# Kernel tuning notes

Hardware: AMD Instinct MI355X
Metric: run time of the kernel (lower is better)

Reference implementation:

```python
import math
import jax, jax.numpy as jnp
import numpy as np

V, D, H, L, F, S, B = 32000, 768, 12, 6, 3072, 2048, 4
DK = D // H


def setup_inputs() -> dict:
    key = jax.random.key(0)
    ks = jax.random.split(key, 16)
    sc = 0.02
    n = jax.random.normal
    inp = {
        "input_ids": jax.random.randint(ks[0], (B, S), 0, V, dtype=jnp.int64)
        if jax.config.jax_enable_x64 else jax.random.randint(ks[0], (B, S), 0, V, dtype=jnp.int32),
        "emb": n(ks[1], (V, D), jnp.float32) * sc,
        "Wq": n(ks[2], (L, D, D), jnp.float32) * sc, "bq": jnp.zeros((L, D), jnp.float32),
        "Wk": n(ks[3], (L, D, D), jnp.float32) * sc, "bk": jnp.zeros((L, D), jnp.float32),
        "Wv": n(ks[4], (L, D, D), jnp.float32) * sc, "bv": jnp.zeros((L, D), jnp.float32),
        "Wo": n(ks[5], (L, D, D), jnp.float32) * sc, "bo": jnp.zeros((L, D), jnp.float32),
        "W1": n(ks[6], (L, D, F), jnp.float32) * sc, "b1": jnp.zeros((L, F), jnp.float32),
        "W2": n(ks[7], (L, F, D), jnp.float32) * sc, "b2": jnp.zeros((L, D), jnp.float32),
        "gamma": jnp.ones((L, D), jnp.float32), "beta": jnp.zeros((L, D), jnp.float32),
    }
    return inp


def _pos_encoding(seq_len, d):
    pos = jnp.arange(seq_len, dtype=jnp.float32)[:, None]                  # [S,1]
    div = jnp.exp(jnp.arange(0, d, 2, dtype=jnp.float32) * (-math.log(10000.0) / d))
    ang = pos * div                                                        # [S,D/2]
    return jnp.stack([jnp.sin(ang), jnp.cos(ang)], axis=-1).reshape(seq_len, d)


def _layernorm(x, g, b, eps=1e-5):
    mu = x.mean(-1, keepdims=True)
    var = ((x - mu) ** 2).mean(-1, keepdims=True)
    return (x - mu) * jax.lax.rsqrt(var + eps) * g + b


def _forward(input_ids, emb, Wq, bq, Wk, bk, Wv, bv, Wo, bo, W1, b1, W2, b2, gamma, beta):
    mask = (input_ids != 1)[:, None, None, :]                              # [B,1,1,S]
    x = emb[input_ids] + _pos_encoding(input_ids.shape[1], emb.shape[1])   # [B,S,D]

    def layer(x, p):
        wq, bq_, wk, bk_, wv, bv_, wo, bo_, w1, b1_, w2, b2_, g, bt = p
        def heads(h):  # [B,S,D] -> [B,H,S,DK]
            return h.reshape(B, S, H, DK).transpose(0, 2, 1, 3)
        q = heads(x @ wq + bq_)
        k = heads(x @ wk + bk_)
        v = heads(x @ wv + bv_)
        scores = jnp.einsum("bhqd,bhkd->bhqk", q, k) / math.sqrt(DK)
        scores = jnp.where(mask, scores, -1e9)
        attn = jax.nn.softmax(scores, axis=-1)
        o = jnp.einsum("bhqk,bhkd->bhqd", attn, v)
        o = o.transpose(0, 2, 1, 3).reshape(B, S, D) @ wo + bo_
        x1 = _layernorm(x + o, g, bt)
        ff = jax.nn.relu(x1 @ w1 + b1_) @ w2 + b2_
        return _layernorm(x1 + ff, g, bt), None  # same norm params reused (as in source)

    x, _ = jax.lax.scan(layer, x, (Wq, bq, Wk, bk, Wv, bv, Wo, bo, W1, b1, W2, b2, gamma, beta))
    return x.mean(axis=1)                                                  # [B,D]


def reference(input_ids, emb, Wq, bq, Wk, bk, Wv, bv, Wo, bo, W1, b1, W2, b2, gamma, beta):
    return _forward(input_ids, emb, Wq, bq, Wk, bk, Wv, bv, Wo, bo, W1, b1, W2, b2, gamma, beta)
```

## Files before the change

### kernel.cpp

```cpp
#include <hip/hip_runtime.h>
#include <hip/hip_bf16.h>
#include <math.h>

typedef unsigned short u16;
typedef unsigned long long u64;
using bf16x8 = __attribute__((ext_vector_type(8))) short;
using f32x4  = __attribute__((ext_vector_type(4))) float;

static constexpr int kD = 768;
static constexpr int kH = 12;
static constexpr int kL = 6;
static constexpr int kF = 3072;
static constexpr int kS = 2048;
static constexpr int kB = 4;
static constexpr int kQW = 2304;
static constexpr int kNT = kB * kS;

__device__ __forceinline__ u16 f2bf(float f) {
    return __bfloat16_as_ushort(__float2bfloat16(f));
}

__device__ __forceinline__ unsigned cvtpk(float a, float b) {
    unsigned d;
    asm volatile("v_cvt_pk_bf16_f32 %0, %1, %2" : "=v"(d) : "v"(a), "v"(b));
    return d;
}

__device__ __forceinline__ void gload16(const void* g, void* l) {
    auto gp = reinterpret_cast<const __attribute__((address_space(1))) unsigned int*>(
        reinterpret_cast<uintptr_t>(g));
    auto lp = reinterpret_cast<__attribute__((address_space(3))) unsigned int*>(
        reinterpret_cast<uintptr_t>(l));
    __builtin_amdgcn_global_load_lds(gp, lp, 16, 0, 0);
}

__global__ __launch_bounds__(256) void embed_pe(
    const int* __restrict__ ids, const float* __restrict__ emb,
    float* __restrict__ x, u16* __restrict__ xbf)
{
    const int t = blockIdx.x;
    const int s = t & (kS - 1);
    const int id = ids[t];
#pragma unroll
    for (int j = 0; j < 3; ++j) {
        const int d = threadIdx.x + (j << 8);
        const float i2 = (float)((d >> 1) << 1);
        const float dv = __expf(i2 * (-9.210340371976184f / 768.f));
        const float ang = (float)s * dv;
        const float pe = (d & 1) ? cosf(ang) : sinf(ang);
        const float v = emb[(size_t)id * kD + d] + pe;
        x[(size_t)t * kD + d] = v;
        if (xbf) xbf[(size_t)t * kD + d] = f2bf(v);
    }
}

__global__ __launch_bounds__(64) void mk_maskbits(const int* __restrict__ ids,
                                                  u64* __restrict__ mbits)
{
    const int w = blockIdx.x;
    const int lane = threadIdx.x;
    const u64 m = __ballot(ids[(size_t)w * 64 + lane] != 1);
    if (lane == 0) mbits[w] = m;
}

__global__ __launch_bounds__(256) void bias_build(
    const float* __restrict__ bq, const float* __restrict__ bk,
    const float* __restrict__ bv, const float* __restrict__ bo,
    const float* __restrict__ b1, const float* __restrict__ b2,
    float* __restrict__ ba)
{
    const int i = blockIdx.x * 256 + threadIdx.x;
    if (i >= 6 * 6912) return;
    const int l = i / 6912, p = i % 6912;
    float v;
    if      (p < 768)  v = bq[l * 768 + p] * 0.125f;
    else if (p < 1536) v = bk[l * 768 + p - 768];
    else if (p < 2304) v = bv[l * 768 + p - 1536];
    else if (p < 3072) v = bo[l * 768 + p - 2304];
    else if (p < 6144) v = b1[(size_t)l * 3072 + p - 3072];
    else               v = b2[l * 768 + p - 6144];
    ba[i] = v;
}

static constexpr size_t OFF_WO = (size_t)2304 * 768;
static constexpr size_t OFF_W1 = OFF_WO + (size_t)768 * 768;
static constexpr size_t OFF_W2 = OFF_W1 + (size_t)3072 * 768;
static constexpr size_t WARENA_E = OFF_W2 + (size_t)768 * 3072;

__global__ __launch_bounds__(256) void cvt_all(
    const float* __restrict__ Wq, const float* __restrict__ Wk,
    const float* __restrict__ Wv, const float* __restrict__ Wo,
    const float* __restrict__ W1, const float* __restrict__ W2,
    u16* __restrict__ wa)
{
    __shared__ float T[64][68];
    const int t = blockIdx.x;
    const float* S; u16* Dp; int Nsrc, Kdst, srow0, scol0; float sc = 1.f;
    if (t < 432) {
        const int ni = t % 36, ki = t / 36;
        const int ng = ni * 64;
        const int sel = ng / 768;
        scol0 = ng % 768; srow0 = ki * 64;
        S = (sel == 0) ? Wq : (sel == 1) ? Wk : Wv;
        if (sel == 0) sc = 0.125f;
        Nsrc = 768; Kdst = 768;
        Dp = wa + (size_t)ng * 768 + srow0;
    } else if (t < 576) {
        const int tt = t - 432; const int ni = tt % 12, ki = tt / 12;
        scol0 = ni * 64; srow0 = ki * 64;
        S = Wo; Nsrc = 768; Kdst = 768;
        Dp = wa + OFF_WO + (size_t)(ni * 64) * 768 + srow0;
    } else if (t < 1152) {
        const int tt = t - 576; const int ni = tt % 48, ki = tt / 48;
        scol0 = ni * 64; srow0 = ki * 64;
        S = W1; Nsrc = 3072; Kdst = 768;
        Dp = wa + OFF_W1 + (size_t)(ni * 64) * 768 + srow0;
    } else {
        const int tt = t - 1152; const int ni = tt % 12, ki = tt / 12;
        scol0 = ni * 64; srow0 = ki * 64;
        S = W2; Nsrc = 768; Kdst = 3072;
        Dp = wa + OFF_W2 + (size_t)(ni * 64) * 3072 + srow0;
    }
    const int tid = threadIdx.x;
#pragma unroll
    for (int i = 0; i < 4; ++i) {
        const int idx = tid + (i << 8);
        const int kr = idx >> 4;
        const int nc = (idx & 15) << 2;
        const float4 v = *(const float4*)(S + (size_t)(srow0 + kr) * Nsrc + scol0 + nc);
        T[kr][nc] = v.x; T[kr][nc + 1] = v.y; T[kr][nc + 2] = v.z; T[kr][nc + 3] = v.w;
    }
    __syncthreads();
#pragma unroll
    for (int i = 0; i < 4; ++i) {
        const int idx = tid + (i << 8);
        const int nr = idx >> 4;
        const int kc = (idx & 15) << 2;
        ushort4 o;
        o.x = f2bf(T[kc][nr] * sc);     o.y = f2bf(T[kc + 1][nr] * sc);
        o.z = f2bf(T[kc + 2][nr] * sc); o.w = f2bf(T[kc + 3][nr] * sc);
        *(ushort4*)(Dp + (size_t)nr * Kdst + kc) = o;
    }
}

__global__ __launch_bounds__(256) void gemm_bf16(
    const u16* __restrict__ A, const u16* __restrict__ Bt,
    const float* __restrict__ bias, void* __restrict__ Cv,
    u16* __restrict__ vTp, int M, int N, int K, int mode)
{
    __shared__ u16 As[2][4096];
    __shared__ u16 Bs[2][4096];
    const int tid = threadIdx.x;
    const int l = tid & 63;
    const int lo = l & 15, hi = l >> 4;
    const int w = tid >> 6, wr = w >> 1, wc = w & 1;

    int brow = blockIdx.x, bcol = blockIdx.y;
    const int gx = gridDim.x;
    if ((gx & 7) == 0) {
        const int id = blockIdx.y * gx + blockIdx.x;
        const int xcd = id & 7, idx = id >> 3;
        const int rpx = gx >> 3;
        brow = xcd * rpx + (idx % rpx);
        bcol = idx / rpx;
    }
    const size_t row0 = (size_t)brow * 128;
    const size_t col0 = (size_t)bcol * 128;

    const int c0 = tid, c1 = tid + 256;
    const int r0 = c0 >> 2, g0 = (c0 & 3) ^ ((r0 >> 1) & 3);
    const int r1 = c1 >> 2, g1 = (c1 & 3) ^ ((r1 >> 1) & 3);
    const u16* a0 = A  + (row0 + r0) * K + g0 * 8;
    const u16* a1 = A  + (row0 + r1) * K + g1 * 8;
    const u16* b0 = Bt + (col0 + r0) * K + g0 * 8;
    const u16* b1 = Bt + (col0 + r1) * K + g1 * 8;

    f32x4 acc[4][4];
#pragma unroll
    for (int i = 0; i < 4; ++i)
#pragma unroll
        for (int j = 0; j < 4; ++j)
#pragma unroll
            for (int r = 0; r < 4; ++r) acc[i][j][r] = 0.f;

    int aoff[4], boff[4];
#pragma unroll
    for (int i = 0; i < 4; ++i) {
        const int ra = wr * 64 + i * 16 + lo;
        aoff[i] = ra * 32 + ((hi ^ ((ra >> 1) & 3)) << 3);
        const int rb = wc * 64 + i * 16 + lo;
        boff[i] = rb * 32 + ((hi ^ ((rb >> 1) & 3)) << 3);
    }

    const int NT = K >> 5;
    gload16(a0, As[0] + c0 * 8);
    gload16(a1, As[0] + c1 * 8);
    gload16(b0, Bs[0] + c0 * 8);
    gload16(b1, Bs[0] + c1 * 8);

    int cur = 0;
    for (int t = 0; t < NT; ++t) {
        if (t + 1 < NT) {
            const int k0 = (t + 1) << 5;
            const int nb = cur ^ 1;
            gload16(a0 + k0, As[nb] + c0 * 8);
            gload16(a1 + k0, As[nb] + c1 * 8);
            gload16(b0 + k0, Bs[nb] + c0 * 8);
            gload16(b1 + k0, Bs[nb] + c1 * 8);
            asm volatile("s_waitcnt vmcnt(4)" ::: "memory");
        } else {
            asm volatile("s_waitcnt vmcnt(0)" ::: "memory");
        }
        __builtin_amdgcn_s_barrier();
        bf16x8 af[4], bfr[4];
#pragma unroll
        for (int i = 0; i < 4; ++i) af[i]  = *(const bf16x8*)&As[cur][aoff[i]];
#pragma unroll
        for (int j = 0; j < 4; ++j) bfr[j] = *(const bf16x8*)&Bs[cur][boff[j]];
#pragma unroll
        for (int i = 0; i < 4; ++i)
#pragma unroll
            for (int j = 0; j < 4; ++j)
                acc[i][j] = __builtin_amdgcn_mfma_f32_16x16x32_bf16(
                    af[i], bfr[j], acc[i][j], 0, 0, 0);
        asm volatile("s_waitcnt lgkmcnt(0)" ::: "memory");
        __builtin_amdgcn_sched_barrier(0);
        __builtin_amdgcn_s_barrier();
        cur ^= 1;
    }

    const bool vmode = (mode == 3) && (col0 >= 1536);
    if (vmode) {
#pragma unroll
        for (int i = 0; i < 4; ++i) {
            const size_t rbase = row0 + wr * 64 + i * 16 + hi * 4;
            const size_t tb = (rbase >> 6) * 64;
            const int k0 = (int)(rbase & 63);
            const int pos = (((k0 >> 2) & 3) << 3) + (((k0 >> 4) & 1) << 2)
                          + ((k0 >> 5) << 5);
#pragma unroll
            for (int j = 0; j < 4; ++j) {
                const size_t c = col0 + wc * 64 + j * 16 + lo;
                const float bs = bias[c];
                const size_t d = c - 1536;
                ushort4 o;
                o.x = f2bf(acc[i][j][0] + bs);
                o.y = f2bf(acc[i][j][1] + bs);
                o.z = f2bf(acc[i][j][2] + bs);
                o.w = f2bf(acc[i][j][3] + bs);
                *(ushort4*)(vTp + d * (size_t)M + tb + pos) = o;
            }
        }
        return;
    }

#pragma unroll
    for (int i = 0; i < 4; ++i) {
        const size_t rbase = row0 + wr * 64 + i * 16 + hi * 4;
#pragma unroll
        for (int j = 0; j < 4; ++j) {
            const size_t c = col0 + wc * 64 + j * 16 + lo;
            const float bs = bias[c];
#pragma unroll
            for (int r = 0; r < 4; ++r) {
                float v = acc[i][j][r] + bs;
                if (mode == 2) v = fmaxf(v, 0.f);
                const size_t off = (rbase + r) * (size_t)N + c;
                if (mode == 0) ((float*)Cv)[off] = v;
                else           ((u16*)Cv)[off]  = f2bf(v);
            }
        }
    }
}

__global__ __launch_bounds__(256) void attn_mfma(
    const u16* __restrict__ QKV, const u16* __restrict__ vT,
    const u64* __restrict__ mbits, u16* __restrict__ O)
{
    __shared__ u16 Ks[2][4096];
    __shared__ u16 Vs[2][4096];

    const int tid = threadIdx.x, l = tid & 63, w = tid >> 6;
    const int lo = l & 15, hi = l >> 4;
    const int h = blockIdx.y, b = blockIdx.z;
    const int q0 = blockIdx.x << 6;

    bf16x8 qf0, qf1;
    {
        const u16* qp = QKV + ((size_t)(b * kS + q0 + w * 16 + lo)) * kQW
                            + h * 64 + hi * 8;
        qf0 = *(const bf16x8*)qp;
        qf1 = *(const bf16x8*)(qp + 32);
    }

    const int ga = tid, gb = tid + 256;
    const int rwA = ga >> 3, sxA = ga & 7, EA = sxA ^ (rwA & 7);
    const int rwB = gb >> 3, sxB = gb & 7, EB = sxB ^ (rwB & 7);
    const u16* Kbase = QKV + (size_t)(b * kS) * kQW + 768 + h * 64;
    const u16* Vbase = vT + (size_t)(h * 64) * kNT + b * kS;

    f32x4 accO[4];
#pragma unroll
    for (int n = 0; n < 4; ++n)
#pragma unroll
        for (int r = 0; r < 4; ++r) accO[n][r] = 0.f;
    float m = -3.0e38f, lsum = 0.f;

    const int ksw = (lo & 7) << 3;
    constexpr int NTt = kS / 64;

    gload16(Kbase + (size_t)rwA * kQW + EA * 8, Ks[0] + ga * 8);
    gload16(Kbase + (size_t)rwB * kQW + EB * 8, Ks[0] + gb * 8);
    gload16(Vbase + (size_t)rwA * kNT + EA * 8, Vs[0] + ga * 8);
    gload16(Vbase + (size_t)rwB * kNT + EB * 8, Vs[0] + gb * 8);

    int cur = 0;
    for (int kt = 0; kt < NTt; ++kt) {
        asm volatile("s_waitcnt vmcnt(0)" ::: "memory");
        __syncthreads();

        if (kt + 1 < NTt) {
            const size_t kof = (size_t)((kt + 1) << 6) * kQW;
            const size_t vof = (size_t)((kt + 1) << 6);
            u16* kd = Ks[cur ^ 1];
            u16* vd = Vs[cur ^ 1];
            gload16(Kbase + kof + (size_t)rwA * kQW + EA * 8, kd + ga * 8);
            gload16(Kbase + kof + (size_t)rwB * kQW + EB * 8, kd + gb * 8);
            gload16(Vbase + (size_t)rwA * kNT + vof + EA * 8, vd + ga * 8);
            gload16(Vbase + (size_t)rwB * kNT + vof + EB * 8, vd + gb * 8);
        }

        f32x4 st[4];
        __builtin_amdgcn_s_setprio(1);
#pragma unroll
        for (int j = 0; j < 4; ++j) {
#pragma unroll
            for (int r = 0; r < 4; ++r) st[j][r] = 0.f;
            const int kb2 = (j * 16 + lo) * 64;
            const bf16x8 k0 = *(const bf16x8*)&Ks[cur][kb2 + ((hi * 8)      ^ ksw)];
            const bf16x8 k1 = *(const bf16x8*)&Ks[cur][kb2 + ((hi * 8 + 32) ^ ksw)];
            st[j] = __builtin_amdgcn_mfma_f32_16x16x32_bf16(k0, qf0, st[j], 0, 0, 0);
            st[j] = __builtin_amdgcn_mfma_f32_16x16x32_bf16(k1, qf1, st[j], 0, 0, 0);
        }
        __builtin_amdgcn_s_setprio(0);

        float rmax = st[0][0];
#pragma unroll
        for (int j = 0; j < 4; ++j)
#pragma unroll
            for (int r = 0; r < 4; ++r) rmax = fmaxf(rmax, st[j][r]);
        rmax = fmaxf(rmax, __shfl_xor(rmax, 16));
        rmax = fmaxf(rmax, __shfl_xor(rmax, 32));

        const bool skip = __all(rmax <= m + 8.0f);
        if (!skip) {
            const float mn = fmaxf(m, rmax);
            const float corr = __expf(m - mn);
            m = mn;
            lsum *= corr;
            float c2[4];
#pragma unroll
            for (int r = 0; r < 4; ++r) c2[r] = __shfl(corr, hi * 4 + r);
#pragma unroll
            for (int n = 0; n < 4; ++n)
#pragma unroll
                for (int r = 0; r < 4; ++r) accO[n][r] *= c2[r];
        }

#pragma unroll
        for (int j = 0; j < 4; ++j)
#pragma unroll
            for (int r = 0; r < 4; ++r) st[j][r] = __expf(st[j][r] - m);

        const u64 mb = mbits[b * 32 + kt];
        if (mb != ~0ull) {
#pragma unroll
            for (int j = 0; j < 4; ++j)
#pragma unroll
                for (int r = 0; r < 4; ++r)
                    if (!((mb >> (j * 16 + hi * 4 + r)) & 1)) st[j][r] = 0.f;
        }

        float ts = 0.f;
#pragma unroll
        for (int j = 0; j < 4; ++j)
#pragma unroll
            for (int r = 0; r < 4; ++r) ts += st[j][r];
        ts += __shfl_xor(ts, 16);
        ts += __shfl_xor(ts, 32);
        lsum += ts;

        union PU { unsigned u[4]; bf16x8 v; } p0, p1;
        p0.u[0] = cvtpk(st[0][0], st[0][1]); p0.u[1] = cvtpk(st[0][2], st[0][3]);
        p0.u[2] = cvtpk(st[1][0], st[1][1]); p0.u[3] = cvtpk(st[1][2], st[1][3]);
        p1.u[0] = cvtpk(st[2][0], st[2][1]); p1.u[1] = cvtpk(st[2][2], st[2][3]);
        p1.u[2] = cvtpk(st[3][0], st[3][1]); p1.u[3] = cvtpk(st[3][2], st[3][3]);

        __builtin_amdgcn_s_setprio(1);
#pragma unroll
        for (int n = 0; n < 4; ++n) {
            const int vb2 = (n * 16 + lo) * 64;
            const bf16x8 v0 = *(const bf16x8*)&Vs[cur][vb2 + ((hi * 8)      ^ ksw)];
            const bf16x8 v1 = *(const bf16x8*)&Vs[cur][vb2 + ((hi * 8 + 32) ^ ksw)];
            accO[n] = __builtin_amdgcn_mfma_f32_16x16x32_bf16(p0.v, v0, accO[n], 0, 0, 0);
            accO[n] = __builtin_amdgcn_mfma_f32_16x16x32_bf16(p1.v, v1, accO[n], 0, 0, 0);
        }
        __builtin_amdgcn_s_setprio(0);
        cur ^= 1;
    }

    float linv[4];
#pragma unroll
    for (int r = 0; r < 4; ++r) linv[r] = 1.f / __shfl(lsum, hi * 4 + r);
#pragma unroll
    for (int n = 0; n < 4; ++n)
#pragma unroll
        for (int r = 0; r < 4; ++r)
            O[((size_t)(b * kS + q0 + w * 16 + hi * 4 + r)) * kD
              + h * 64 + n * 16 + lo] = f2bf(accO[n][r] * linv[r]);
}

__global__ __launch_bounds__(256) void add_ln(
    const float* __restrict__ a, const float* __restrict__ r,
    const float* __restrict__ g, const float* __restrict__ bt,
    float* __restrict__ out, u16* __restrict__ outb)
{
    const int lane = threadIdx.x & 63;
    const size_t row = (size_t)blockIdx.x * 4 + (threadIdx.x >> 6);
    const float4* a4 = (const float4*)(a + row * kD);
    const float4* r4 = (const float4*)(r + row * kD);
    float4 v[3];
    float s = 0.f;
#pragma unroll
    for (int j = 0; j < 3; ++j) {
        const float4 av = a4[j * 64 + lane];
        const float4 rv = r4[j * 64 + lane];
        v[j].x = av.x + rv.x; v[j].y = av.y + rv.y;
        v[j].z = av.z + rv.z; v[j].w = av.w + rv.w;
        s += v[j].x + v[j].y + v[j].z + v[j].w;
    }
#pragma unroll
    for (int off = 32; off; off >>= 1) s += __shfl_xor(s, off);
    const float mu = s * (1.f / 768.f);
    float vs = 0.f;
#pragma unroll
    for (int j = 0; j < 3; ++j) {
        float t0 = v[j].x - mu, t1 = v[j].y - mu, t2 = v[j].z - mu, t3 = v[j].w - mu;
        vs = fmaf(t0, t0, fmaf(t1, t1, fmaf(t2, t2, fmaf(t3, t3, vs))));
    }
#pragma unroll
    for (int off = 32; off; off >>= 1) vs += __shfl_xor(vs, off);
    const float rstd = rsqrtf(vs * (1.f / 768.f) + 1e-5f);
    const float4* g4 = (const float4*)g;
    const float4* b4 = (const float4*)bt;
#pragma unroll
    for (int j = 0; j < 3; ++j) {
        const float4 gv = g4[j * 64 + lane];
        const float4 bv = b4[j * 64 + lane];
        float4 o;
        o.x = (v[j].x - mu) * rstd * gv.x + bv.x;
        o.y = (v[j].y - mu) * rstd * gv.y + bv.y;
        o.z = (v[j].z - mu) * rstd * gv.z + bv.z;
        o.w = (v[j].w - mu) * rstd * gv.w + bv.w;
        ((float4*)(out + row * kD))[j * 64 + lane] = o;
        if (outb) {
            ushort4 ob4;
            ob4.x = f2bf(o.x); ob4.y = f2bf(o.y);
            ob4.z = f2bf(o.z); ob4.w = f2bf(o.w);
            ((ushort4*)(outb + row * kD))[j * 64 + lane] = ob4;
        }
    }
}

__global__ __launch_bounds__(256) void mean_part(
    const float* __restrict__ x, float* __restrict__ mred)
{
    const int c = blockIdx.x, b = blockIdx.y;
    const int tid = threadIdx.x;
    const float* base = x + ((size_t)b * kS + c * 32) * kD;
#pragma unroll
    for (int j = 0; j < 3; ++j) {
        const int d = tid + (j << 8);
        float s = 0.f;
#pragma unroll 8
        for (int t = 0; t < 32; ++t) s += base[(size_t)t * kD + d];
        mred[((size_t)b * 64 + c) * kD + d] = s;
    }
}

__global__ __launch_bounds__(256) void mean_fin(
    const float* __restrict__ mred, float* __restrict__ out)
{
    const int d = blockIdx.x * 256 + threadIdx.x;
    const int b = blockIdx.y;
    float s = 0.f;
#pragma unroll
    for (int c = 0; c < 64; ++c) s += mred[((size_t)b * 64 + c) * kD + d];
    out[b * kD + d] = s * (1.f / 2048.f);
}

__global__ __launch_bounds__(256) void mean_s(
    const float* __restrict__ x, float* __restrict__ out)
{
    const int d = blockIdx.x * 256 + threadIdx.x;
    const int b = blockIdx.y;
    float s = 0.f;
    for (int t = 0; t < kS; ++t) s += x[((size_t)b * kS + t) * kD + d];
    out[b * kD + d] = s * (1.f / 2048.f);
}

__global__ __launch_bounds__(256) void gemm_f32(
    const float* __restrict__ A, const float* __restrict__ W,
    const float* __restrict__ bias, float* __restrict__ C,
    int M, int N, int K, int relu)
{
    __shared__ float As[16][68];
    __shared__ float Bs[16][68];
    const int tid = threadIdx.x;
    const int row0 = blockIdx.x << 6;
    const int col0 = blockIdx.y << 6;
    const int tx = tid & 15, ty = tid >> 4;
    const int ar = tid >> 2;
    const int ak = (tid & 3) << 2;
    const int bk = tid >> 4;
    const int bc = (tid & 15) << 2;
    float acc[4][4] = {};
    const float* Ap = A + (size_t)(row0 + ar) * K + ak;
    const float* Wp = W + (size_t)bk * N + col0 + bc;
    for (int k0 = 0; k0 < K; k0 += 16) {
        const float4 a4 = *(const float4*)(Ap + k0);
        const float4 b4 = *(const float4*)(Wp + (size_t)k0 * N);
        __syncthreads();
        As[ak + 0][ar] = a4.x; As[ak + 1][ar] = a4.y;
        As[ak + 2][ar] = a4.z; As[ak + 3][ar] = a4.w;
        *(float4*)&Bs[bk][bc] = b4;
        __syncthreads();
#pragma unroll
        for (int kk = 0; kk < 16; ++kk) {
            const float4 av = *(const float4*)&As[kk][ty << 2];
            const float4 bv = *(const float4*)&Bs[kk][tx << 2];
            const float aa[4] = {av.x, av.y, av.z, av.w};
            const float bb[4] = {bv.x, bv.y, bv.z, bv.w};
#pragma unroll
            for (int i = 0; i < 4; ++i)
#pragma unroll
                for (int j = 0; j < 4; ++j)
                    acc[i][j] = fmaf(aa[i], bb[j], acc[i][j]);
        }
    }
#pragma unroll
    for (int i = 0; i < 4; ++i) {
        const int row = row0 + (ty << 2) + i;
#pragma unroll
        for (int j = 0; j < 4; ++j) {
            const int col = col0 + (tx << 2) + j;
            float v = acc[i][j] + bias[col];
            if (relu) v = fmaxf(v, 0.f);
            C[(size_t)row * N + col] = v;
        }
    }
}

__global__ __launch_bounds__(256) void attn_fused(
    const float* __restrict__ Q, const float* __restrict__ Km,
    const float* __restrict__ Vm, const int* __restrict__ ids,
    float* __restrict__ O)
{
    __shared__ float Ksf[64 * 64];
    __shared__ float Vtf[64 * 64];
    __shared__ float Qs[16][64];
    __shared__ float Psf[4][4][64];
    const int tid = threadIdx.x;
    const int w = tid >> 6;
    const int lane = tid & 63;
    const int h = blockIdx.y, b = blockIdx.z;
    const int qrow0 = blockIdx.x << 4;
    {
        const int r = tid >> 4;
        const int c4 = tid & 15;
        const float4 q4 = *(const float4*)(
            Q + ((size_t)(b * kS + qrow0 + r)) * kD + h * 64 + (c4 << 2));
        Qs[r][(c4 << 2) + 0] = q4.x * 0.125f;
        Qs[r][(c4 << 2) + 1] = q4.y * 0.125f;
        Qs[r][(c4 << 2) + 2] = q4.z * 0.125f;
        Qs[r][(c4 << 2) + 3] = q4.w * 0.125f;
    }
    float m[4], lsum[4], o[4];
#pragma unroll
    for (int r = 0; r < 4; ++r) { m[r] = -3.0e38f; lsum[r] = 0.f; o[r] = 0.f; }
    for (int kt = 0; kt < kS / 64; ++kt) {
        __syncthreads();
#pragma unroll
        for (int i = 0; i < 4; ++i) {
            const int lin = tid + (i << 8);
            const int row = lin >> 4;
            const int s4 = lin & 15;
            const size_t gro = ((size_t)(b * kS + (kt << 6) + row)) * kD + h * 64 + (s4 << 2);
            const float4 k4 = *(const float4*)(Km + gro);
            ((float4*)Ksf)[(row << 4) + (s4 ^ (row & 7))] = k4;
            const float4 v4 = *(const float4*)(Vm + gro);
            const int ksl = row >> 2, ke = row & 3;
            const int d0 = s4 << 2;
            Vtf[(d0 + 0) * 64 + ((ksl ^ ((d0 + 0) & 7)) << 2) + ke] = v4.x;
            Vtf[(d0 + 1) * 64 + ((ksl ^ ((d0 + 1) & 7)) << 2) + ke] = v4.y;
            Vtf[(d0 + 2) * 64 + ((ksl ^ ((d0 + 2) & 7)) << 2) + ke] = v4.z;
            Vtf[(d0 + 3) * 64 + ((ksl ^ ((d0 + 3) & 7)) << 2) + ke] = v4.w;
        }
        __syncthreads();
        const bool masked = (ids[(size_t)b * kS + (kt << 6) + lane] == 1);
        float scr[4] = {0.f, 0.f, 0.f, 0.f};
#pragma unroll
        for (int i16 = 0; i16 < 16; ++i16) {
            const float4 kv = ((const float4*)Ksf)[(lane << 4) + (i16 ^ (lane & 7))];
#pragma unroll
            for (int r = 0; r < 4; ++r) {
                const float4 qv = *(const float4*)&Qs[(w << 2) + r][i16 << 2];
                scr[r] = fmaf(kv.x, qv.x, fmaf(kv.y, qv.y,
                          fmaf(kv.z, qv.z, fmaf(kv.w, qv.w, scr[r]))));
            }
        }
#pragma unroll
        for (int r = 0; r < 4; ++r) {
            float sm = masked ? -3.0e38f : scr[r];
#pragma unroll
            for (int off = 32; off; off >>= 1) sm = fmaxf(sm, __shfl_xor(sm, off));
            const float mn = fmaxf(m[r], sm);
            const float cr = __expf(m[r] - mn);
            const float pv = masked ? 0.f : __expf(scr[r] - mn);
            float ps = pv;
#pragma unroll
            for (int off = 32; off; off >>= 1) ps += __shfl_xor(ps, off);
            lsum[r] = lsum[r] * cr + ps;
            o[r] *= cr;
            m[r] = mn;
            Psf[w][r][lane] = pv;
        }
#pragma unroll
        for (int i16 = 0; i16 < 16; ++i16) {
            const float4 vv = ((const float4*)Vtf)[(lane << 4) + (i16 ^ (lane & 7))];
#pragma unroll
            for (int r = 0; r < 4; ++r) {
                const float4 pv = *(const float4*)&Psf[w][r][i16 << 2];
                o[r] = fmaf(pv.x, vv.x, fmaf(pv.y, vv.y,
                        fmaf(pv.z, vv.z, fmaf(pv.w, vv.w, o[r]))));
            }
        }
    }
#pragma unroll
    for (int r = 0; r < 4; ++r)
        O[((size_t)(b * kS + qrow0 + (w << 2) + r)) * kD + h * 64 + lane] =
            o[r] / lsum[r];
}

extern "C" void kernel_launch(void* const* d_in, const int* in_sizes, int n_in,
                              void* d_out, int out_size, void* d_ws, size_t ws_size,
                              hipStream_t stream)
{
    const int*   ids   = (const int*)  d_in[0];
    const float* emb   = (const float*)d_in[1];
    const float* Wq    = (const float*)d_in[2];
    const float* bq    = (const float*)d_in[3];
    const float* Wk    = (const float*)d_in[4];
    const float* bk    = (const float*)d_in[5];
    const float* Wv    = (const float*)d_in[6];
    const float* bv    = (const float*)d_in[7];
    const float* Wo    = (const float*)d_in[8];
    const float* bo    = (const float*)d_in[9];
    const float* W1    = (const float*)d_in[10];
    const float* b1    = (const float*)d_in[11];
    const float* W2    = (const float*)d_in[12];
    const float* b2    = (const float*)d_in[13];
    const float* gamma = (const float*)d_in[14];
    const float* beta  = (const float*)d_in[15];
    float* out = (float*)d_out;

    const size_t BUFE = (size_t)kB * kS * kD;
    const size_t WDD  = (size_t)kD * kD;
    const size_t WDF  = (size_t)kD * kF;
    const size_t HIDE = (size_t)kB * kS * kF;
    const int NTOK = kB * kS;

    const size_t NEED = BUFE * 4 * 2
                      + BUFE * 2
                      + HIDE * 2
                      + WARENA_E * 2
                      + (size_t)6 * 6912 * 4
                      + 128 * 8
                      + (size_t)kB * 64 * kD * 4;

    if (ws_size >= NEED) {
        float* xb  = (float*)d_ws;
        float* ob  = xb + BUFE;
        u16*   abf = (u16*)(ob + BUFE);
        u16*   sc  = abf + BUFE;
        u16*   vtb = sc + (size_t)NTOK * kQW;
        u16*   wa  = sc + HIDE;
        float* ba  = (float*)(wa + WARENA_E);
        u64*   mbt = (u64*)(ba + 6 * 6912);
        float* mrd = (float*)(mbt + 128);

        embed_pe<<<NTOK, 256, 0, stream>>>(ids, emb, xb, abf);
        mk_maskbits<<<kB * kS / 64, 64, 0, stream>>>(ids, mbt);
        bias_build<<<(6 * 6912 + 255) / 256, 256, 0, stream>>>(
            bq, bk, bv, bo, b1, b2, ba);

        for (int l = 0; l < kL; ++l) {
            const size_t oDD = (size_t)l * WDD;
            const size_t oDF = (size_t)l * WDF;
            const float* bl = ba + (size_t)l * 6912;
            const float* gl  = gamma + (size_t)l * kD;
            const float* btl = beta  + (size_t)l * kD;

            cvt_all<<<1728, 256, 0, stream>>>(
                Wq + oDD, Wk + oDD, Wv + oDD, Wo + oDD, W1 + oDF, W2 + oDF, wa);

            gemm_bf16<<<dim3(64, 18), 256, 0, stream>>>(
                abf, wa, bl, sc, vtb, NTOK, kQW, kD, 3);

            attn_mfma<<<dim3(kS / 64, kH, kB), 256, 0, stream>>>(
                sc, vtb, mbt, abf);

            gemm_bf16<<<dim3(64, 6), 256, 0, stream>>>(
                abf, wa + OFF_WO, bl + 2304, ob, nullptr, NTOK, kD, kD, 0);

            add_ln<<<NTOK / 4, 256, 0, stream>>>(xb, ob, gl, btl, ob, abf);

            gemm_bf16<<<dim3(64, 24), 256, 0, stream>>>(
                abf, wa + OFF_W1, bl + 3072, sc, nullptr, NTOK, kF, kD, 2);
            gemm_bf16<<<dim3(64, 6), 256, 0, stream>>>(
                sc, wa + OFF_W2, bl + 6144, xb, nullptr, NTOK, kD, kF, 0);

            add_ln<<<NTOK / 4, 256, 0, stream>>>(ob, xb, gl, btl, xb, abf);
        }

        mean_part<<<dim3(64, kB), 256, 0, stream>>>(xb, mrd);
        mean_fin<<<dim3(kD / 256, kB), 256, 0, stream>>>(mrd, out);
        return;
    }

    if (ws_size < 5 * BUFE * sizeof(float)) return;
    float* xb = (float*)d_ws;
    float* kb = xb + BUFE;
    float* qb = kb + BUFE;
    float* vb = qb + BUFE;
    float* obf = vb + BUFE;
    float* hb = qb;

    embed_pe<<<NTOK, 256, 0, stream>>>(ids, emb, xb, nullptr);
    for (int l = 0; l < kL; ++l) {
        const size_t oDD = (size_t)l * WDD;
        const size_t oDF = (size_t)l * WDF;
        gemm_f32<<<dim3(NTOK / 64, kD / 64), 256, 0, stream>>>(
            xb, Wq + oDD, bq + (size_t)l * kD, qb, NTOK, kD, kD, 0);
        gemm_f32<<<dim3(NTOK / 64, kD / 64), 256, 0, stream>>>(
            xb, Wk + oDD, bk + (size_t)l * kD, kb, NTOK, kD, kD, 0);
        gemm_f32<<<dim3(NTOK / 64, kD / 64), 256, 0, stream>>>(
            xb, Wv + oDD, bv + (size_t)l * kD, vb, NTOK, kD, kD, 0);
        attn_fused<<<dim3(kS / 16, kH, kB), 256, 0, stream>>>(qb, kb, vb, ids, obf);
        gemm_f32<<<dim3(NTOK / 64, kD / 64), 256, 0, stream>>>(
            obf, Wo + oDD, bo + (size_t)l * kD, qb, NTOK, kD, kD, 0);
        add_ln<<<NTOK / 4, 256, 0, stream>>>(xb, qb,
            gamma + (size_t)l * kD, beta + (size_t)l * kD, kb, nullptr);
        for (int c = 0; c < 2; ++c) {
            const size_t ro = (size_t)c * 4096;
            gemm_f32<<<dim3(4096 / 64, kF / 64), 256, 0, stream>>>(
                kb + ro * kD, W1 + oDF, b1 + (size_t)l * kF, hb, 4096, kF, kD, 1);
            gemm_f32<<<dim3(4096 / 64, kD / 64), 256, 0, stream>>>(
                hb, W2 + oDF, b2 + (size_t)l * kD, obf + ro * kD, 4096, kD, kF, 0);
        }
        add_ln<<<NTOK / 4, 256, 0, stream>>>(kb, obf,
            gamma + (size_t)l * kD, beta + (size_t)l * kD, xb, nullptr);
    }
    mean_s<<<dim3(kD / 256, kB), 256, 0, stream>>>(xb, out);
}
```

Measured before the change: 1.757 ms.

## Keep residual stream in bf16 and use exp2 softmax with folded log2e scale

The fast path now holds the residual stream, the GEMM outputs and the LayerNorm inputs and outputs in bf16 instead of fp32, which cuts global memory traffic in add_ln and in the Wo/W2 GEMM epilogues. The 1/sqrt(dk)*log2(e) factor is folded into Wq/bq so attention can use a native exp2 instead of expf, and the rescale-skip threshold is widened to match the base-2 domain. Keeping the residual in bf16 accumulates rounding error across six layers and may hurt accuracy against the fp32 reference.

New measurement: 1.662 ms. -5.4%, faster.

```diff
diff --git a/kernel.cpp b/kernel.cpp
--- a/kernel.cpp
+++ b/kernel.cpp
@@ -16,14 +16,25 @@
 static constexpr int kQW = 2304;
 static constexpr int kNT = kB * kS;
 
+static constexpr float kQScale = 0.18033688011112043f;
+
 __device__ __forceinline__ u16 f2bf(float f) {
     return __bfloat16_as_ushort(__float2bfloat16(f));
 }
-
+__device__ __forceinline__ float b2f(u16 u) {
+    return __uint_as_float((unsigned)u << 16);
+}
 __device__ __forceinline__ unsigned cvtpk(float a, float b) {
     unsigned d;
     asm volatile("v_cvt_pk_bf16_f32 %0, %1, %2" : "=v"(d) : "v"(a), "v"(b));
     return d;
+}
+__device__ __forceinline__ float exp2fast(float x) {
+#if __has_builtin(__builtin_amdgcn_exp2f)
+    return __builtin_amdgcn_exp2f(x);
+#else
+    return __expf(x * 0.6931471805599453f);
+#endif
 }
 
 __device__ __forceinline__ void gload16(const void* g, void* l) {
@@ -36,7 +47,7 @@
 
 __global__ __launch_bounds__(256) void embed_pe(
     const int* __restrict__ ids, const float* __restrict__ emb,
-    float* __restrict__ x, u16* __restrict__ xbf)
+    u16* __restrict__ xbf)
 {
     const int t = blockIdx.x;
     const int s = t & (kS - 1);
@@ -48,9 +59,25 @@
         const float dv = __expf(i2 * (-9.210340371976184f / 768.f));
         const float ang = (float)s * dv;
         const float pe = (d & 1) ? cosf(ang) : sinf(ang);
-        const float v = emb[(size_t)id * kD + d] + pe;
-        x[(size_t)t * kD + d] = v;
-        if (xbf) xbf[(size_t)t * kD + d] = f2bf(v);
+        xbf[(size_t)t * kD + d] = f2bf(emb[(size_t)id * kD + d] + pe);
+    }
+}
+
+__global__ __launch_bounds__(256) void embed_pe_f32(
+    const int* __restrict__ ids, const float* __restrict__ emb,
+    float* __restrict__ x)
+{
+    const int t = blockIdx.x;
+    const int s = t & (kS - 1);
+    const int id = ids[t];
+#pragma unroll
+    for (int j = 0; j < 3; ++j) {
+        const int d = threadIdx.x + (j << 8);
+        const float i2 = (float)((d >> 1) << 1);
+        const float dv = __expf(i2 * (-9.210340371976184f / 768.f));
+        const float ang = (float)s * dv;
+        const float pe = (d & 1) ? cosf(ang) : sinf(ang);
+        x[(size_t)t * kD + d] = emb[(size_t)id * kD + d] + pe;
     }
 }
 
@@ -73,7 +100,7 @@
     if (i >= 6 * 6912) return;
     const int l = i / 6912, p = i % 6912;
     float v;
-    if      (p < 768)  v = bq[l * 768 + p] * 0.125f;
+    if      (p < 768)  v = bq[l * 768 + p] * kQScale;
     else if (p < 1536) v = bk[l * 768 + p - 768];
     else if (p < 2304) v = bv[l * 768 + p - 1536];
     else if (p < 3072) v = bo[l * 768 + p - 2304];
@@ -102,7 +129,7 @@
         const int sel = ng / 768;
         scol0 = ng % 768; srow0 = ki * 64;
         S = (sel == 0) ? Wq : (sel == 1) ? Wk : Wv;
-        if (sel == 0) sc = 0.125f;
+        if (sel == 0) sc = kQScale;
         Nsrc = 768; Kdst = 768;
         Dp = wa + (size_t)ng * 768 + srow0;
     } else if (t < 576) {
@@ -265,9 +292,7 @@
             for (int r = 0; r < 4; ++r) {
                 float v = acc[i][j][r] + bs;
                 if (mode == 2) v = fmaxf(v, 0.f);
-                const size_t off = (rbase + r) * (size_t)N + c;
-                if (mode == 0) ((float*)Cv)[off] = v;
-                else           ((u16*)Cv)[off]  = f2bf(v);
+                ((u16*)Cv)[(rbase + r) * (size_t)N + c] = f2bf(v);
             }
         }
     }
@@ -352,10 +377,10 @@
         rmax = fmaxf(rmax, __shfl_xor(rmax, 16));
         rmax = fmaxf(rmax, __shfl_xor(rmax, 32));
 
-        const bool skip = __all(rmax <= m + 8.0f);
+        const bool skip = __all(rmax <= m + 11.0f);
         if (!skip) {
             const float mn = fmaxf(m, rmax);
-            const float corr = __expf(m - mn);
+            const float corr = exp2fast(m - mn);
             m = mn;
             lsum *= corr;
             float c2[4];
@@ -370,7 +395,7 @@
 #pragma unroll
         for (int j = 0; j < 4; ++j)
 #pragma unroll
-            for (int r = 0; r < 4; ++r) st[j][r] = __expf(st[j][r] - m);
+            for (int r = 0; r < 4; ++r) st[j][r] = exp2fast(st[j][r] - m);
 
         const u64 mb = mbits[b * 32 + kt];
         if (mb != ~0ull) {
@@ -420,10 +445,87 @@
               + h * 64 + n * 16 + lo] = f2bf(accO[n][r] * linv[r]);
 }
 
-__global__ __launch_bounds__(256) void add_ln(
+__global__ __launch_bounds__(256) void add_ln_bf(
+    const u16* __restrict__ a, const u16* __restrict__ r,
+    const float* __restrict__ g, const float* __restrict__ bt,
+    u16* __restrict__ out)
+{
+    const int lane = threadIdx.x & 63;
+    const size_t row = (size_t)blockIdx.x * 4 + (threadIdx.x >> 6);
+    const ushort4* a4 = (const ushort4*)(a + row * kD);
+    const ushort4* r4 = (const ushort4*)(r + row * kD);
+    float v[3][4];
+    float s = 0.f;
+#pragma unroll
+    for (int j = 0; j < 3; ++j) {
+        const ushort4 av = a4[j * 64 + lane];
+        const ushort4 rv = r4[j * 64 + lane];
+        v[j][0] = b2f(av.x) + b2f(rv.x);
+        v[j][1] = b2f(av.y) + b2f(rv.y);
+        v[j][2] = b2f(av.z) + b2f(rv.z);
+        v[j][3] = b2f(av.w) + b2f(rv.w);
+        s += v[j][0] + v[j][1] + v[j][2] + v[j][3];
+    }
+#pragma unroll
+    for (int off = 32; off; off >>= 1) s += __shfl_xor(s, off);
+    const float mu = s * (1.f / 768.f);
+    float vs = 0.f;
+#pragma unroll
+    for (int j = 0; j < 3; ++j)
+#pragma unroll
+        for (int e = 0; e < 4; ++e) {
+            const float t0 = v[j][e] - mu;
+            vs = fmaf(t0, t0, vs);
+        }
+#pragma unroll
+    for (int off = 32; off; off >>= 1) vs += __shfl_xor(vs, off);
+    const float rstd = rsqrtf(vs * (1.f / 768.f) + 1e-5f);
+    const float4* g4 = (const float4*)g;
+    const float4* b4 = (const float4*)bt;
+#pragma unroll
+    for (int j = 0; j < 3; ++j) {
+        const float4 gv = g4[j * 64 + lane];
+        const float4 bv = b4[j * 64 + lane];
+        ushort4 o;
+        o.x = f2bf((v[j][0] - mu) * rstd * gv.x + bv.x);
+        o.y = f2bf((v[j][1] - mu) * rstd * gv.y + bv.y);
+        o.z = f2bf((v[j][2] - mu) * rstd * gv.z + bv.z);
+        o.w = f2bf((v[j][3] - mu) * rstd * gv.w + bv.w);
+        ((ushort4*)(out + row * kD))[j * 64 + lane] = o;
+    }
+}
+
+__global__ __launch_bounds__(192) void mean_part_bf(
+    const u16* __restrict__ x, float* __restrict__ mred)
+{
+    const int c = blockIdx.x, b = blockIdx.y;
+    const int d = threadIdx.x * 4;
+    const u16* base = x + ((size_t)b * kS + c * 32) * kD + d;
+    float s0 = 0.f, s1 = 0.f, s2 = 0.f, s3 = 0.f;
+#pragma unroll 8
+    for (int t = 0; t < 32; ++t) {
+        const ushort4 u = *(const ushort4*)(base + (size_t)t * kD);
+        s0 += b2f(u.x); s1 += b2f(u.y); s2 += b2f(u.z); s3 += b2f(u.w);
+    }
+    float4 o; o.x = s0; o.y = s1; o.z = s2; o.w = s3;
+    *(float4*)(mred + ((size_t)b * 64 + c) * kD + d) = o;
+}
+
+__global__ __launch_bounds__(256) void mean_fin(
+    const float* __restrict__ mred, float* __restrict__ out)
+{
+    const int d = blockIdx.x * 256 + threadIdx.x;
+    const int b = blockIdx.y;
+    float s = 0.f;
+#pragma unroll
+    for (int c = 0; c < 64; ++c) s += mred[((size_t)b * 64 + c) * kD + d];
+    out[b * kD + d] = s * (1.f / 2048.f);
+}
+
+__global__ __launch_bounds__(256) void add_ln_f32(
     const float* __restrict__ a, const float* __restrict__ r,
     const float* __restrict__ g, const float* __restrict__ bt,
-    float* __restrict__ out, u16* __restrict__ outb)
+    float* __restrict__ out)
 {
     const int lane = threadIdx.x & 63;
     const size_t row = (size_t)blockIdx.x * 4 + (threadIdx.x >> 6);
@@ -463,40 +565,7 @@
         o.z = (v[j].z - mu) * rstd * gv.z + bv.z;
         o.w = (v[j].w - mu) * rstd * gv.w + bv.w;
         ((float4*)(out + row * kD))[j * 64 + lane] = o;
-        if (outb) {
-            ushort4 ob4;
-            ob4.x = f2bf(o.x); ob4.y = f2bf(o.y);
-            ob4.z = f2bf(o.z); ob4.w = f2bf(o.w);
-            ((ushort4*)(outb + row * kD))[j * 64 + lane] = ob4;
-        }
-    }
-}
-
-__global__ __launch_bounds__(256) void mean_part(
-    const float* __restrict__ x, float* __restrict__ mred)
-{
-    const int c = blockIdx.x, b = blockIdx.y;
-    const int tid = threadIdx.x;
-    const float* base = x + ((size_t)b * kS + c * 32) * kD;
-#pragma unroll
-    for (int j = 0; j < 3; ++j) {
-        const int d = tid + (j << 8);
-        float s = 0.f;
-#pragma unroll 8
-        for (int t = 0; t < 32; ++t) s += base[(size_t)t * kD + d];
-        mred[((size_t)b * 64 + c) * kD + d] = s;
-    }
-}
-
-__global__ __launch_bounds__(256) void mean_fin(
-    const float* __restrict__ mred, float* __restrict__ out)
-{
-    const int d = blockIdx.x * 256 + threadIdx.x;
-    const int b = blockIdx.y;
-    float s = 0.f;
-#pragma unroll
-    for (int c = 0; c < 64; ++c) s += mred[((size_t)b * 64 + c) * kD + d];
-    out[b * kD + d] = s * (1.f / 2048.f);
+    }
 }
 
 __global__ __launch_bounds__(256) void mean_s(
@@ -680,8 +749,7 @@
     const size_t HIDE = (size_t)kB * kS * kF;
     const int NTOK = kB * kS;
 
-    const size_t NEED = BUFE * 4 * 2
-                      + BUFE * 2
+    const size_t NEED = BUFE * 2 * 4
                       + HIDE * 2
                       + WARENA_E * 2
                       + (size_t)6 * 6912 * 4
@@ -689,17 +757,18 @@
                       + (size_t)kB * 64 * kD * 4;
 
     if (ws_size >= NEED) {
-        float* xb  = (float*)d_ws;
-        float* ob  = xb + BUFE;
-        u16*   abf = (u16*)(ob + BUFE);
-        u16*   sc  = abf + BUFE;
+        u16*   xb  = (u16*)d_ws;
+        u16*   x1b = xb + BUFE;
+        u16*   ao  = x1b + BUFE;
+        u16*   ob  = ao + BUFE;
+        u16*   sc  = ob + BUFE;
         u16*   vtb = sc + (size_t)NTOK * kQW;
         u16*   wa  = sc + HIDE;
         float* ba  = (float*)(wa + WARENA_E);
         u64*   mbt = (u64*)(ba + 6 * 6912);
         float* mrd = (float*)(mbt + 128);
 
-        embed_pe<<<NTOK, 256, 0, stream>>>(ids, emb, xb, abf);
+        embed_pe<<<NTOK, 256, 0, stream>>>(ids, emb, xb);
         mk_maskbits<<<kB * kS / 64, 64, 0, stream>>>(ids, mbt);
         bias_build<<<(6 * 6912 + 255) / 256, 256, 0, stream>>>(
             bq, bk, bv, bo, b1, b2, ba);
@@ -715,25 +784,25 @@
                 Wq + oDD, Wk + oDD, Wv + oDD, Wo + oDD, W1 + oDF, W2 + oDF, wa);
 
             gemm_bf16<<<dim3(64, 18), 256, 0, stream>>>(
-                abf, wa, bl, sc, vtb, NTOK, kQW, kD, 3);
+                xb, wa, bl, sc, vtb, NTOK, kQW, kD, 3);
 
             attn_mfma<<<dim3(kS / 64, kH, kB), 256, 0, stream>>>(
-                sc, vtb, mbt, abf);
+                sc, vtb, mbt, ao);
 
             gemm_bf16<<<dim3(64, 6), 256, 0, stream>>>(
-                abf, wa + OFF_WO, bl + 2304, ob, nullptr, NTOK, kD, kD, 0);
-
-            add_ln<<<NTOK / 4, 256, 0, stream>>>(xb, ob, gl, btl, ob, abf);
+                ao, wa + OFF_WO, bl + 2304, ob, nullptr, NTOK, kD, kD, 1);
+
+            add_ln_bf<<<NTOK / 4, 256, 0, stream>>>(xb, ob, gl, btl, x1b);
 
             gemm_bf16<<<dim3(64, 24), 256, 0, stream>>>(
-                abf, wa + OFF_W1, bl + 3072, sc, nullptr, NTOK, kF, kD, 2);
+                x1b, wa + OFF_W1, bl + 3072, sc, nullptr, NTOK, kF, kD, 2);
             gemm_bf16<<<dim3(64, 6), 256, 0, stream>>>(
-                sc, wa + OFF_W2, bl + 6144, xb, nullptr, NTOK, kD, kF, 0);
-
-            add_ln<<<NTOK / 4, 256, 0, stream>>>(ob, xb, gl, btl, xb, abf);
-        }
-
-        mean_part<<<dim3(64, kB), 256, 0, stream>>>(xb, mrd);
+                sc, wa + OFF_W2, bl + 6144, ob, nullptr, NTOK, kD, kF, 1);
+
+            add_ln_bf<<<NTOK / 4, 256, 0, stream>>>(x1b, ob, gl, btl, xb);
+        }
+
+        mean_part_bf<<<dim3(64, kB), 192, 0, stream>>>(xb, mrd);
         mean_fin<<<dim3(kD / 256, kB), 256, 0, stream>>>(mrd, out);
         return;
     }
@@ -746,7 +815,7 @@
     float* obf = vb + BUFE;
     float* hb = qb;
 
-    embed_pe<<<NTOK, 256, 0, stream>>>(ids, emb, xb, nullptr);
+    embed_pe_f32<<<NTOK, 256, 0, stream>>>(ids, emb, xb);
     for (int l = 0; l < kL; ++l) {
         const size_t oDD = (size_t)l * WDD;
         const size_t oDF = (size_t)l * WDF;
@@ -759,8 +828,8 @@
         attn_fused<<<dim3(kS / 16, kH, kB), 256, 0, stream>>>(qb, kb, vb, ids, obf);
         gemm_f32<<<dim3(NTOK / 64, kD / 64), 256, 0, stream>>>(
             obf, Wo + oDD, bo + (size_t)l * kD, qb, NTOK, kD, kD, 0);
-        add_ln<<<NTOK / 4, 256, 0, stream>>>(xb, qb,
-            gamma + (size_t)l * kD, beta + (size_t)l * kD, kb, nullptr);
+        add_ln_f32<<<NTOK / 4, 256, 0, stream>>>(xb, qb,
+            gamma + (size_t)l * kD, beta + (size_t)l * kD, kb);
         for (int c = 0; c < 2; ++c) {
             const size_t ro = (size_t)c * 4096;
             gemm_f32<<<dim3(4096 / 64, kF / 64), 256, 0, stream>>>(
@@ -768,8 +837,8 @@
             gemm_f32<<<dim3(4096 / 64, kD / 64), 256, 0, stream>>>(
                 hb, W2 + oDF, b2 + (size_t)l * kD, obf + ro * kD, 4096, kD, kF, 0);
         }
-        add_ln<<<NTOK / 4, 256, 0, stream>>>(kb, obf,
-            gamma + (size_t)l * kD, beta + (size_t)l * kD, xb, nullptr);
+        add_ln_f32<<<NTOK / 4, 256, 0, stream>>>(kb, obf,
+            gamma + (size_t)l * kD, beta + (size_t)l * kD, xb);
     }
     mean_s<<<dim3(kD / 256, kB), 256, 0, stream>>>(xb, out);
 }
```
